# Optimization experiments

Hardware: AMD Instinct MI355X
Metric: run time of the kernel (lower is better)

## Reference

```python
import jax, jax.numpy as jnp
import numpy as np

NUM_GROUPS = 32
EPS = 1e-6


def group_norm(x, gamma, beta):
    # x: [B, C, H, W]
    b, c, h, w = x.shape
    xg = x.reshape(b, NUM_GROUPS, c // NUM_GROUPS, h, w)
    mean = xg.mean(axis=(2, 3, 4), keepdims=True)
    var = xg.var(axis=(2, 3, 4), keepdims=True)
    xn = ((xg - mean) * jax.lax.rsqrt(var + EPS)).reshape(b, c, h, w)
    return xn * gamma[None, :, None, None] + beta[None, :, None, None]


def setup_inputs() -> dict:
    key = jax.random.key(0)
    ks = jax.random.split(key, 10)
    B, C, H, W = 2, 512, 64, 64
    s = 1.0 / np.sqrt(C)
    return {
        "x": jax.random.normal(ks[0], (B, C, H, W), dtype=jnp.float32),
        "gamma": jnp.ones((C,), jnp.float32),
        "beta": jnp.zeros((C,), jnp.float32),
        "Wq": jax.random.normal(ks[1], (C, C), jnp.float32) * s,
        "bq": jnp.zeros((C,), jnp.float32),
        "Wk": jax.random.normal(ks[2], (C, C), jnp.float32) * s,
        "bk": jnp.zeros((C,), jnp.float32),
        "Wv": jax.random.normal(ks[3], (C, C), jnp.float32) * s,
        "bv": jnp.zeros((C,), jnp.float32),
        "Wo": jax.random.normal(ks[4], (C, C), jnp.float32) * s,
        "bo": jnp.zeros((C,), jnp.float32),
    }


def reference(x, gamma, beta, Wq, bq, Wk, bk, Wv, bv, Wo, bo):
    b, c, h, w = x.shape
    hn = group_norm(x, gamma, beta)               # [B,C,H,W]
    hf = hn.reshape(b, c, h * w)                  # [B,C,N]
    # 1x1 convs == channel matmuls
    q = jnp.einsum('oc,bcn->bon', Wq, hf) + bq[None, :, None]
    k = jnp.einsum('oc,bcn->bon', Wk, hf) + bk[None, :, None]
    v = jnp.einsum('oc,bcn->bon', Wv, hf) + bv[None, :, None]
    scale = float(c) ** -0.5
    scores = jnp.einsum('bci,bcj->bij', q, k) * scale   # [B,N,N]
    attn = jax.nn.softmax(scores, axis=-1)
    out = jnp.einsum('bij,bcj->bci', attn, v)            # [B,C,N]
    out = jnp.einsum('oc,bcn->bon', Wo, out) + bo[None, :, None]
    return x + out.reshape(b, c, h, w)
```

## Files before the change

### kernel.cpp

```cpp
#include <hip/hip_runtime.h>

#define BB 2
#define CC 512
#define NS 4096
#define NGROUP 32
#define TILE 128
#define RSTRIDE 132

typedef __bf16 bf16_8 __attribute__((ext_vector_type(8)));
typedef __bf16 bf16_4 __attribute__((ext_vector_type(4)));
typedef float f32_4 __attribute__((ext_vector_type(4)));

#define SMEM_BYTES 65536
#define SMEM256 131072

__device__ __forceinline__ void gld_lds16(const __bf16* g, __bf16* l) {
  __builtin_amdgcn_global_load_lds(
      (const __attribute__((address_space(1))) unsigned int*)g,
      (__attribute__((address_space(3))) unsigned int*)l, 16, 0, 0);
}

__global__ __launch_bounds__(256) void gn_stats(const float* __restrict__ x,
                                                float* __restrict__ stats) {
  const float4* p = (const float4*)(x + (size_t)blockIdx.x * 65536);
  float s = 0.f, q = 0.f;
  for (int i = threadIdx.x; i < 16384; i += 256) {
    float4 v = p[i];
    s += v.x + v.y + v.z + v.w;
    q += v.x * v.x + v.y * v.y + v.z * v.z + v.w * v.w;
  }
#pragma unroll
  for (int off = 32; off > 0; off >>= 1) {
    s += __shfl_down(s, off, 64);
    q += __shfl_down(q, off, 64);
  }
  __shared__ float ls[4], lq[4];
  int wave = threadIdx.x >> 6, lane = threadIdx.x & 63;
  if (lane == 0) { ls[wave] = s; lq[wave] = q; }
  __syncthreads();
  if (threadIdx.x == 0) {
    float S = ls[0] + ls[1] + ls[2] + ls[3];
    float Q = lq[0] + lq[1] + lq[2] + lq[3];
    float mean = S * (1.f / 65536.f);
    float var = Q * (1.f / 65536.f) - mean * mean;
    stats[blockIdx.x * 2] = mean;
    stats[blockIdx.x * 2 + 1] = rsqrtf(var + 1e-6f);
  }
}

__global__ __launch_bounds__(256) void gn_apply_t(const float* __restrict__ x,
                                                  const float* __restrict__ stats,
                                                  const float* __restrict__ gamma,
                                                  const float* __restrict__ beta,
                                                  __bf16* __restrict__ hnT) {
  __shared__ float tile[32][33];
  int b = blockIdx.z;
  int c0 = blockIdx.y * 32;
  int n0 = blockIdx.x * 32;
  int tx = threadIdx.x;
  int ty = threadIdx.y;
  const float* xb = x + (size_t)b * CC * NS;
#pragma unroll
  for (int i = 0; i < 4; i++) {
    int c = c0 + ty + i * 8;
    float mean = stats[(b * NGROUP + (c >> 4)) * 2 + 0];
    float rstd = stats[(b * NGROUP + (c >> 4)) * 2 + 1];
    float v = xb[(size_t)c * NS + n0 + tx];
    tile[ty + i * 8][tx] = (v - mean) * rstd * gamma[c] + beta[c];
  }
  __syncthreads();
  __bf16* out = hnT + (size_t)b * NS * CC;
#pragma unroll
  for (int i = 0; i < 4; i++) {
    int n = n0 + ty + i * 8;
    out[(size_t)n * CC + c0 + tx] = (__bf16)tile[tx][ty + i * 8];
  }
}

__global__ __launch_bounds__(256) void cvt_w(const float* __restrict__ w0, const float* __restrict__ w1,
                                             const float* __restrict__ w2, const float* __restrict__ w3,
                                             __bf16* __restrict__ o0, __bf16* __restrict__ o1,
                                             __bf16* __restrict__ o2, __bf16* __restrict__ o3) {
  int tsel = blockIdx.x >> 8;
  int i = (blockIdx.x & 255) * 256 + threadIdx.x;
  const float* src = tsel == 0 ? w0 : tsel == 1 ? w1 : tsel == 2 ? w2 : w3;
  __bf16* dst = tsel == 0 ? o0 : tsel == 1 ? o1 : tsel == 2 ? o2 : o3;
  float4 v = ((const float4*)src)[i];
  bf16_4 r;
  r[0] = (__bf16)v.x; r[1] = (__bf16)v.y; r[2] = (__bf16)v.z; r[3] = (__bf16)v.w;
  ((bf16_4*)dst)[i] = r;
}

__device__ __forceinline__ void gemm_core8(const __bf16* __restrict__ A, const __bf16* __restrict__ B,
                                           int K, int lda, int ldb,
                                           __bf16* lds, f32_4 (&acc)[4][2]) {
  const int t = threadIdx.x;
  const int lane = t & 63;
  const int wave = t >> 6;
  const int lrow = lane & 15, quad = lane >> 4;
  const int wrow = (wave >> 2) * 64, wcol = (wave & 3) * 32;
  const int co = (quad ^ ((lrow >> 1) & 3)) * 8;
  const int r0 = t >> 2;
  const int kp = ((t & 3) ^ ((t >> 3) & 3)) * 8;
  const __bf16* pA = A + (size_t)r0 * lda + kp;
  const __bf16* pB = B + (size_t)r0 * ldb + kp;
  {
    __bf16* lA = lds;
    __bf16* lB = lds + 8192;
    gld_lds16(pA,      &lA[t * 8]);
    gld_lds16(pA + 32, &lA[4096 + t * 8]);
    gld_lds16(pB,      &lB[t * 8]);
    gld_lds16(pB + 32, &lB[4096 + t * 8]);
  }
  int buf = 0;
  for (int k0 = 0; k0 < K; k0 += 64, buf ^= 1) {
    __syncthreads();
    if (k0 + 64 < K) {
      __bf16* lA = lds + (buf ^ 1) * 16384;
      __bf16* lB = lA + 8192;
      gld_lds16(pA + k0 + 64, &lA[t * 8]);
      gld_lds16(pA + k0 + 96, &lA[4096 + t * 8]);
      gld_lds16(pB + k0 + 64, &lB[t * 8]);
      gld_lds16(pB + k0 + 96, &lB[4096 + t * 8]);
    }
    const __bf16* bA = lds + buf * 16384;
    const __bf16* bB = bA + 8192;
#pragma unroll
    for (int ks = 0; ks < 2; ks++) {
      const __bf16* la = bA + ks * 4096;
      const __bf16* lb = bB + ks * 4096;
      bf16_8 af[4], bfr[2];
#pragma unroll
      for (int i = 0; i < 4; i++)
        af[i] = *(const bf16_8*)&la[(wrow + i * 16 + lrow) * 32 + co];
#pragma unroll
      for (int j = 0; j < 2; j++)
        bfr[j] = *(const bf16_8*)&lb[(wcol + j * 16 + lrow) * 32 + co];
#pragma unroll
      for (int i = 0; i < 4; i++)
#pragma unroll
        for (int j = 0; j < 2; j++)
          acc[i][j] = __builtin_amdgcn_mfma_f32_16x16x32_bf16(af[i], bfr[j], acc[i][j], 0, 0, 0);
    }
  }
}

__device__ __forceinline__ void stage_acc8(float* ls, const f32_4 (&acc)[4][2], int pass) {
  const int t = threadIdx.x;
  const int lane = t & 63, wave = t >> 6;
  const int lrow = lane & 15, quad = lane >> 4;
  const int wrow = (wave >> 2) * 64, wcol = (wave & 3) * 32;
  if ((wrow >> 6) == pass) {
#pragma unroll
    for (int i = 0; i < 4; i++)
#pragma unroll
      for (int r = 0; r < 4; r++)
#pragma unroll
        for (int jj = 0; jj < 2; jj++)
          ls[(i * 16 + quad * 4 + r) * RSTRIDE + wcol + jj * 16 + lrow] = acc[i][jj][r];
  }
}

__device__ __forceinline__ void drain_bf16_8(const float* ls, __bf16* gdst, int ldg) {
  const int t = threadIdx.x;
#pragma unroll
  for (int k2 = 0; k2 < 4; k2++) {
    int idx = k2 * 512 + t;
    int row = idx >> 5, col = (idx & 31) * 4;
    f32_4 v = *(const f32_4*)&ls[row * RSTRIDE + col];
    bf16_4 o;
    o[0] = (__bf16)v[0]; o[1] = (__bf16)v[1]; o[2] = (__bf16)v[2]; o[3] = (__bf16)v[3];
    *(bf16_4*)&gdst[(size_t)row * ldg + col] = o;
  }
}

__device__ __forceinline__ void gemm_core256(const __bf16* __restrict__ A,
                                             const __bf16* __restrict__ B,
                                             int K, int lda, int ldb,
                                             __bf16* lds, f32_4 (&acc)[8][4]) {
  const int t = threadIdx.x;
  const int lane = t & 63;
  const int wave = t >> 6;
  const int lrow = lane & 15, quad = lane >> 4;
  const int wm = wave >> 2, wn = wave & 3;
  const int r0 = t >> 2;
  const int kp = ((t & 3) ^ ((t >> 3) & 3)) * 8;
  const __bf16* gA0 = A + (size_t)r0 * lda + kp;
  const __bf16* gA1 = A + (size_t)(r0 + 128) * lda + kp;
  const __bf16* gB0 = B + (size_t)r0 * ldb + kp;
  const __bf16* gB1 = B + (size_t)(r0 + 128) * ldb + kp;
  const int co = (quad ^ ((lrow >> 1) & 3)) * 8;
  const int aoff = (wm * 128 + lrow) * 32 + co;
  const int boff = 16384 + (wn * 64 + lrow) * 32 + co;
  const int KT = K >> 6;

#define STG(bufv, isB, srcp, hh, ktv)                                         \
  {                                                                           \
    __bf16* d_ = lds + (bufv) * 32768 + (isB) * 16384 + (hh) * 4096 + t * 8;  \
    const __bf16* s_ = (srcp) + (ktv) * 64;                                   \
    gld_lds16(s_, d_);                                                        \
    gld_lds16(s_ + 32, d_ + 8192);                                            \
  }
#define LOAD_AF(IH)                                                           \
  _Pragma("unroll") for (int i = 0; i < 4; i++)                               \
      _Pragma("unroll") for (int ks = 0; ks < 2; ks++)                        \
          af[i][ks] = *(const bf16_8*)&bb[aoff + ((IH) * 4 + i) * 512 + ks * 8192];
#define LOAD_BV(J0)                                                           \
  _Pragma("unroll") for (int j = 0; j < 2; j++)                               \
      _Pragma("unroll") for (int ks = 0; ks < 2; ks++)                        \
          bv[(J0) + j][ks] = *(const bf16_8*)&bb[boff + ((J0) + j) * 512 + ks * 8192];
#define MFMA16(I0, J0)                                                        \
  _Pragma("unroll") for (int ks = 0; ks < 2; ks++)                            \
      _Pragma("unroll") for (int i = 0; i < 4; i++)                           \
          _Pragma("unroll") for (int j = 0; j < 2; j++)                       \
              acc[(I0) + i][(J0) + j] = __builtin_amdgcn_mfma_f32_16x16x32_bf16( \
                  af[i][ks], bv[(J0) + j][ks], acc[(I0) + i][(J0) + j], 0, 0, 0);
#define PHASE_BEGIN()                                                         \
  __builtin_amdgcn_s_barrier();                                               \
  asm volatile("s_waitcnt lgkmcnt(0)" ::: "memory");                          \
  __builtin_amdgcn_sched_barrier(0);                                          \
  __builtin_amdgcn_s_setprio(1);
#define PHASE_END()                                                           \
  __builtin_amdgcn_s_setprio(0);                                              \
  __builtin_amdgcn_s_barrier();

  STG(0, 0, gA0, 0, 0)
  STG(0, 0, gA1, 1, 0)
  STG(0, 1, gB0, 0, 0)
  STG(0, 1, gB1, 1, 0)
  STG(1, 1, gB0, 0, 1)
  STG(1, 1, gB1, 1, 1)
  asm volatile("s_waitcnt vmcnt(4)" ::: "memory");
  __builtin_amdgcn_s_barrier();

  for (int it = 0; it < (KT >> 1); ++it) {
#pragma unroll
    for (int h = 0; h < 2; ++h) {
      const int kt = 2 * it + h;
      const __bf16* bb = lds + h * 32768;
      bf16_8 af[4][2], bv[4][2];
      LOAD_AF(0)
      LOAD_BV(0)
      if (kt + 1 < KT) STG(h ^ 1, 0, gA0, 0, kt + 1)
      PHASE_BEGIN()
      MFMA16(0, 0)
      PHASE_END()
      LOAD_BV(2)
      if (kt + 1 < KT) STG(h ^ 1, 0, gA1, 1, kt + 1)
      PHASE_BEGIN()
      MFMA16(0, 2)
      PHASE_END()
      LOAD_AF(1)
      if (kt + 2 < KT) STG(h, 1, gB0, 0, kt + 2)
      PHASE_BEGIN()
      MFMA16(4, 0)
      PHASE_END()
      if (kt + 2 < KT) STG(h, 1, gB1, 1, kt + 2)
      PHASE_BEGIN()
      MFMA16(4, 2)
      __builtin_amdgcn_s_setprio(0);
      if (kt + 2 < KT) {
        asm volatile("s_waitcnt vmcnt(4)" ::: "memory");
      } else {
        asm volatile("s_waitcnt vmcnt(0)" ::: "memory");
      }
      __builtin_amdgcn_s_barrier();
    }
  }
#undef STG
#undef LOAD_AF
#undef LOAD_BV
#undef MFMA16
#undef PHASE_BEGIN
#undef PHASE_END
}

__global__ __launch_bounds__(512, 2) void e_gemm256(const __bf16* __restrict__ qT,
                                                    const __bf16* __restrict__ kT,
                                                    __bf16* __restrict__ E,
                                                    float* __restrict__ l,
                                                    float scale) {
  extern __shared__ __bf16 ldsdyn[];
  const int bid = blockIdx.x;
  const int lin = (bid & 7) * 64 + (bid >> 3);
  const int b = lin >> 8;
  const int rm = lin & 255;
  const int R = rm >> 5, s = rm & 31;
  const int mt = (R >> 2) * 8 + (s >> 2);
  const int nt = (R & 3) * 4 + (s & 3);
  const int m0 = mt * 256, n0 = nt * 256;
  const long long sBNC = (long long)NS * CC;
  const long long sBNN = (long long)NS * NS;
  const __bf16* Ap = qT + (size_t)b * sBNC + (size_t)m0 * CC;
  const __bf16* Bp = kT + (size_t)b * sBNC + (size_t)n0 * CC;

  f32_4 acc[8][4];
#pragma unroll
  for (int i = 0; i < 8; i++)
#pragma unroll
    for (int j = 0; j < 4; j++) acc[i][j] = {0.f, 0.f, 0.f, 0.f};

  gemm_core256(Ap, Bp, CC, CC, CC, ldsdyn, acc);

  const int t = threadIdx.x;
  const int lane = t & 63, wave = t >> 6;
  const int lrow = lane & 15, quad = lane >> 4;
  const int wm = wave >> 2, wn = wave & 3;
  __bf16* Ep = E + (size_t)b * sBNN;
  float* lp = l + (size_t)b * NS;
#pragma unroll
  for (int i = 0; i < 8; i++) {
#pragma unroll
    for (int r = 0; r < 4; r++) {
      int gm = m0 + wm * 128 + i * 16 + quad * 4 + r;
      float rp = 0.f;
#pragma unroll
      for (int j = 0; j < 4; j++) {
        int gn = n0 + wn * 64 + j * 16 + lrow;
        float ev = __expf(acc[i][j][r] * scale);
        rp += ev;
        Ep[(size_t)gm * NS + gn] = (__bf16)ev;
      }
      rp += __shfl_down(rp, 8, 16);
      rp += __shfl_down(rp, 4, 16);
      rp += __shfl_down(rp, 2, 16);
      rp += __shfl_down(rp, 1, 16);
      if (lrow == 0) atomicAdd(&lp[gm], rp);
    }
  }
}

__global__ __launch_bounds__(512, 2) void ao256(const __bf16* __restrict__ E,
                                                const __bf16* __restrict__ vv,
                                                __bf16* __restrict__ p0,
                                                __bf16* __restrict__ p1,
                                                __bf16* __restrict__ p2,
                                                __bf16* __restrict__ p3) {
  extern __shared__ __bf16 ldsdyn[];
  const int bid = blockIdx.x;
  const int lin = (bid & 7) * 32 + (bid >> 3);
  const int split = lin >> 6;
  const int rem = lin & 63;
  const int b = rem >> 5;
  const int mt = (rem & 31) >> 1;
  const int nt = rem & 1;
  const int m0 = mt * 256, n0 = nt * 256;
  const long long sBNN = (long long)NS * NS;
  const long long sBCN = (long long)CC * NS;
  const long long sBNC = (long long)NS * CC;
  const __bf16* Ap = E + (size_t)b * sBNN + (size_t)m0 * NS + (size_t)split * 1024;
  const __bf16* Bp = vv + (size_t)b * sBCN + (size_t)n0 * NS + (size_t)split * 1024;
  __bf16* Cp = (split == 0 ? p0 : split == 1 ? p1 : split == 2 ? p2 : p3) + (size_t)b * sBNC;

  f32_4 acc[8][4];
#pragma unroll
  for (int i = 0; i < 8; i++)
#pragma unroll
    for (int j = 0; j < 4; j++) acc[i][j] = {0.f, 0.f, 0.f, 0.f};

  gemm_core256(Ap, Bp, 1024, NS, NS, ldsdyn, acc);

  const int t = threadIdx.x;
  const int lane = t & 63, wave = t >> 6;
  const int lrow = lane & 15, quad = lane >> 4;
  const int wm = wave >> 2, wn = wave & 3;
#pragma unroll
  for (int i = 0; i < 8; i++) {
#pragma unroll
    for (int r = 0; r < 4; r++) {
      int gm = m0 + wm * 128 + i * 16 + quad * 4 + r;
#pragma unroll
      for (int j = 0; j < 4; j++) {
        int gn = n0 + wn * 64 + j * 16 + lrow;
        Cp[(size_t)gm * CC + gn] = (__bf16)acc[i][j][r];
      }
    }
  }
}

__global__ __launch_bounds__(512, 4) void qkv_gemm(const __bf16* __restrict__ hnT,
                                                   const __bf16* __restrict__ Wq,
                                                   const __bf16* __restrict__ Wk,
                                                   const __bf16* __restrict__ Wv,
                                                   const float* __restrict__ bq,
                                                   const float* __restrict__ bk,
                                                   const float* __restrict__ bv,
                                                   __bf16* __restrict__ qT,
                                                   __bf16* __restrict__ kT,
                                                   __bf16* __restrict__ vv) {
  __shared__ char smem[SMEM_BYTES];
  __bf16* lds = (__bf16*)smem;
  float* lsr = (float*)smem;
  const int b = blockIdx.z;
  const int id = blockIdx.x;
  const int sel = id >> 7;
  const int r = id & 127;
  const long long sBNC = (long long)NS * CC;
  const long long sBCN = (long long)CC * NS;

  int m0, n0, N;
  const __bf16 *Ap, *Bp;
  __bf16* Cp;
  const float* bias;
  if (sel < 2) {
    m0 = (r >> 2) * TILE;
    n0 = (r & 3) * TILE;
    Ap = hnT + (size_t)b * sBNC + (size_t)m0 * CC;
    Bp = (sel == 0 ? Wq : Wk) + (size_t)n0 * CC;
    Cp = (sel == 0 ? qT : kT) + (size_t)b * sBNC;
    bias = (sel == 0 ? bq : bk);
    N = CC;
  } else {
    m0 = (r & 3) * TILE;
    n0 = (r >> 2) * TILE;
    Ap = Wv + (size_t)m0 * CC;
    Bp = hnT + (size_t)b * sBNC + (size_t)n0 * CC;
    Cp = vv + (size_t)b * sBCN;
    bias = bv;
    N = NS;
  }

  f32_4 acc[4][2];
#pragma unroll
  for (int i = 0; i < 4; i++)
#pragma unroll
    for (int j = 0; j < 2; j++) acc[i][j] = {0.f, 0.f, 0.f, 0.f};

  gemm_core8(Ap, Bp, CC, CC, CC, lds, acc);

  const int t = threadIdx.x;
  const int lane = t & 63;
  const int lrow = lane & 15, quad = lane >> 4;
  const int wave = t >> 6;
  const int wrow = (wave >> 2) * 64, wcol = (wave & 3) * 32;
#pragma unroll
  for (int i = 0; i < 4; i++)
#pragma unroll
    for (int r2 = 0; r2 < 4; r2++) {
      float rowb = (sel == 2) ? bias[m0 + wrow + i * 16 + quad * 4 + r2] : 0.f;
#pragma unroll
      for (int j = 0; j < 2; j++) {
        float cb = (sel < 2) ? bias[n0 + wcol + j * 16 + lrow] : rowb;
        acc[i][j][r2] += cb;
      }
    }

#pragma unroll
  for (int p = 0; p < 2; p++) {
    __syncthreads();
    stage_acc8(lsr, acc, p);
    __syncthreads();
    drain_bf16_8(lsr, Cp + (size_t)(m0 + p * 64) * N + n0, N);
  }
}

__global__ __launch_bounds__(256) void reduce_ao4(const __bf16* __restrict__ p0,
                                                  const __bf16* __restrict__ p1,
                                                  const __bf16* __restrict__ p2,
                                                  const __bf16* __restrict__ p3,
                                                  const float* __restrict__ l,
                                                  __bf16* __restrict__ o) {
  int i = blockIdx.x * 256 + threadIdx.x;
  int row = i >> 6;
  float inv = 1.f / l[row];
  bf16_8 a = ((const bf16_8*)p0)[i];
  bf16_8 c = ((const bf16_8*)p1)[i];
  bf16_8 d = ((const bf16_8*)p2)[i];
  bf16_8 e = ((const bf16_8*)p3)[i];
  bf16_8 r;
#pragma unroll
  for (int k = 0; k < 8; k++)
    r[k] = (__bf16)(((float)a[k] + (float)c[k] + (float)d[k] + (float)e[k]) * inv);
  ((bf16_8*)o)[i] = r;
}

__global__ __launch_bounds__(512, 4) void wo_split(const __bf16* __restrict__ Wo,
                                                   const __bf16* __restrict__ aoT,
                                                   __bf16* __restrict__ pw0,
                                                   __bf16* __restrict__ pw1) {
  __shared__ char smem[SMEM_BYTES];
  __bf16* lds = (__bf16*)smem;
  float* lsr = (float*)smem;
  const int b = blockIdx.z & 1;
  const int split = blockIdx.z >> 1;
  const int m0 = blockIdx.y * TILE;
  const int n0 = blockIdx.x * TILE;
  const long long sBNC = (long long)NS * CC;
  const long long sBCN = (long long)CC * NS;
  const __bf16* Ap = Wo + (size_t)m0 * CC + (size_t)split * 256;
  const __bf16* Bp = aoT + (size_t)b * sBNC + (size_t)n0 * CC + (size_t)split * 256;
  __bf16* Cp = (split ? pw1 : pw0) + (size_t)b * sBCN;

  f32_4 acc[4][2];
#pragma unroll
  for (int i = 0; i < 4; i++)
#pragma unroll
    for (int j = 0; j < 2; j++) acc[i][j] = {0.f, 0.f, 0.f, 0.f};

  gemm_core8(Ap, Bp, 256, CC, CC, lds, acc);

#pragma unroll
  for (int p = 0; p < 2; p++) {
    __syncthreads();
    stage_acc8(lsr, acc, p);
    __syncthreads();
    drain_bf16_8(lsr, Cp + (size_t)(m0 + p * 64) * NS + n0, NS);
  }
}

__global__ __launch_bounds__(256) void final_out(const __bf16* __restrict__ pw0,
                                                 const __bf16* __restrict__ pw1,
                                                 const float* __restrict__ bo,
                                                 const float* __restrict__ x,
                                                 float* __restrict__ out) {
  int i = blockIdx.x * 256 + threadIdx.x;
  int o = (i >> 10) & (CC - 1);
  float bias = bo[o];
  bf16_4 a = ((const bf16_4*)pw0)[i];
  bf16_4 c = ((const bf16_4*)pw1)[i];
  float4 xr = ((const float4*)x)[i];
  float4 r;
  r.x = (float)a[0] + (float)c[0] + bias + xr.x;
  r.y = (float)a[1] + (float)c[1] + bias + xr.y;
  r.z = (float)a[2] + (float)c[2] + bias + xr.z;
  r.w = (float)a[3] + (float)c[3] + bias + xr.w;
  ((float4*)out)[i] = r;
}

extern "C" void kernel_launch(void* const* d_in, const int* in_sizes, int n_in,
                              void* d_out, int out_size, void* d_ws, size_t ws_size,
                              hipStream_t stream) {
  const float* x = (const float*)d_in[0];
  const float* gamma = (const float*)d_in[1];
  const float* beta = (const float*)d_in[2];
  const float* Wq = (const float*)d_in[3];
  const float* bq = (const float*)d_in[4];
  const float* Wk = (const float*)d_in[5];
  const float* bk = (const float*)d_in[6];
  const float* Wv = (const float*)d_in[7];
  const float* bv = (const float*)d_in[8];
  const float* Wo = (const float*)d_in[9];
  const float* bo = (const float*)d_in[10];
  float* out = (float*)d_out;

  char* ws = (char*)d_ws;
  __bf16* hnT = (__bf16*)(ws + 0);
  __bf16* qT  = (__bf16*)(ws + 8388608);
  __bf16* kT  = (__bf16*)(ws + 16777216);
  __bf16* vv  = (__bf16*)(ws + 25165824);
  __bf16* aoT = (__bf16*)(ws + 33554432);
  __bf16* Eb  = (__bf16*)(ws + 41943040);
  __bf16* pw0 = (__bf16*)(ws + 41943040);
  __bf16* pw1 = (__bf16*)(ws + 50331648);
  __bf16* Wqb = (__bf16*)(ws + 109051904);
  __bf16* Wkb = (__bf16*)(ws + 109576192);
  __bf16* Wvb = (__bf16*)(ws + 110100480);
  __bf16* Wob = (__bf16*)(ws + 110624768);
  float* stats = (float*)(ws + 111149056);
  float* lsum = (float*)(ws + 109051904);
  __bf16* p0 = hnT;
  __bf16* p1 = qT;
  __bf16* p2 = kT;
  __bf16* p3 = aoT;

  const float scale = 0.044194173824159216f;

  static int smem_attr_set = 0;
  if (!smem_attr_set) {
    hipFuncSetAttribute(reinterpret_cast<const void*>(e_gemm256),
                        hipFuncAttributeMaxDynamicSharedMemorySize, SMEM256);
    hipFuncSetAttribute(reinterpret_cast<const void*>(ao256),
                        hipFuncAttributeMaxDynamicSharedMemorySize, SMEM256);
    smem_attr_set = 1;
  }

  cvt_w<<<1024, 256, 0, stream>>>(Wq, Wk, Wv, Wo, Wqb, Wkb, Wvb, Wob);
  gn_stats<<<BB * NGROUP, 256, 0, stream>>>(x, stats);
  gn_apply_t<<<dim3(NS / 32, CC / 32, BB), dim3(32, 8), 0, stream>>>(x, stats, gamma, beta, hnT);

  qkv_gemm<<<dim3(384, 1, BB), 512, 0, stream>>>(hnT, Wqb, Wkb, Wvb, bq, bk, bv, qT, kT, vv);

  hipMemsetAsync(lsum, 0, BB * NS * sizeof(float), stream);
  e_gemm256<<<512, 512, SMEM256, stream>>>(qT, kT, Eb, lsum, scale);

  ao256<<<256, 512, SMEM256, stream>>>(Eb, vv, p0, p1, p2, p3);
  reduce_ao4<<<2048, 256, 0, stream>>>(p0, p1, p2, p3, lsum, aoT);

  wo_split<<<dim3(NS / TILE, CC / TILE, 2 * BB), 512, 0, stream>>>(Wob, aoT, pw0, pw1);
  final_out<<<4096, 256, 0, stream>>>(pw0, pw1, bo, x, out);
}
```

Measured before the change: 246.8 us.

## Use persistent two-tile E-GEMM blocks with a new K-split pipelined core

The score GEMM launches 256 blocks instead of 512. Each block computes two 256x256 output tiles that share the same Q row tile. A new GEMM core splits each 64-wide K step into two 32-wide sub-phases with double-buffered LDS and per-sub-phase barriers. This halves the block count to match the two-blocks-per-CU occupancy, so the whole grid fits in a single wave, and it spreads LDS loads across finer phases. The cost is fewer blocks, which means less latency hiding and serialised per-tile epilogues inside each block.

Result: slower. 258.4 us (+4.7%).

```diff
diff --git a/kernel.cpp b/kernel.cpp
--- a/kernel.cpp
+++ b/kernel.cpp
@@ -275,6 +275,88 @@
 #undef PHASE_END
 }
 
+__device__ __forceinline__ void gemm_core256v2(const __bf16* __restrict__ A,
+                                               const __bf16* __restrict__ B,
+                                               int K, int lda, int ldb,
+                                               __bf16* lds, f32_4 (&acc)[8][4]) {
+  const int t = threadIdx.x;
+  const int lane = t & 63;
+  const int wave = t >> 6;
+  const int lrow = lane & 15, quad = lane >> 4;
+  const int wm = wave >> 2, wn = wave & 3;
+  const int r0 = t >> 2;
+  const int kp = ((t & 3) ^ ((t >> 3) & 3)) * 8;
+  const __bf16* gA0 = A + (size_t)r0 * lda + kp;
+  const __bf16* gA1 = A + (size_t)(r0 + 128) * lda + kp;
+  const __bf16* gB0 = B + (size_t)r0 * ldb + kp;
+  const __bf16* gB1 = B + (size_t)(r0 + 128) * ldb + kp;
+  const int co = (quad ^ ((lrow >> 1) & 3)) * 8;
+  const int aoff = (wm * 128 + lrow) * 32 + co;
+  const int boff = 16384 + (wn * 64 + lrow) * 32 + co;
+  const int KT = K >> 6;
+
+#define STG4(bufv, ktv, ks)                                                    \
+  {                                                                            \
+    __bf16* dA = lds + (bufv) * 32768 + (ks) * 8192 + t * 8;                   \
+    __bf16* dB = dA + 16384;                                                   \
+    const int goff = (ktv) * 64 + (ks) * 32;                                   \
+    gld_lds16(gA0 + goff, dA);                                                 \
+    gld_lds16(gA1 + goff, dA + 4096);                                          \
+    gld_lds16(gB0 + goff, dB);                                                 \
+    gld_lds16(gB1 + goff, dB + 4096);                                          \
+  }
+#define LOAD_AF8(ks)                                                           \
+  _Pragma("unroll") for (int f = 0; f < 8; f++)                                \
+      af8[f] = *(const bf16_8*)&bb[aoff + f * 512 + (ks) * 8192];
+#define LOAD_BV4(ks)                                                           \
+  _Pragma("unroll") for (int j = 0; j < 4; j++)                                \
+      bv4[j] = *(const bf16_8*)&bb[boff + j * 512 + (ks) * 8192];
+#define MFMA32()                                                               \
+  _Pragma("unroll") for (int f = 0; f < 8; f++)                                \
+      _Pragma("unroll") for (int j = 0; j < 4; j++)                            \
+          acc[f][j] = __builtin_amdgcn_mfma_f32_16x16x32_bf16(                 \
+              af8[f], bv4[j], acc[f][j], 0, 0, 0);
+#define PHASE2(h, kt, ks)                                                      \
+  {                                                                            \
+    const __bf16* bb = lds + (h) * 32768;                                      \
+    bf16_8 af8[8], bv4[4];                                                     \
+    LOAD_AF8(ks)                                                               \
+    LOAD_BV4(ks)                                                               \
+    if ((kt) + 1 < KT) STG4((h) ^ 1, (kt) + 1, ks)                             \
+    asm volatile("s_waitcnt lgkmcnt(8)" ::: "memory");                         \
+    __builtin_amdgcn_s_barrier();                                              \
+    asm volatile("s_waitcnt lgkmcnt(0)" ::: "memory");                         \
+    __builtin_amdgcn_sched_barrier(0);                                         \
+    __builtin_amdgcn_s_setprio(1);                                             \
+    MFMA32()                                                                   \
+    __builtin_amdgcn_s_setprio(0);                                             \
+    if ((kt) + 1 < KT) {                                                       \
+      asm volatile("s_waitcnt vmcnt(4)" ::: "memory");                         \
+    } else if ((ks) == 0) {                                                    \
+      asm volatile("s_waitcnt vmcnt(0)" ::: "memory");                         \
+    }                                                                          \
+    __builtin_amdgcn_s_barrier();                                              \
+  }
+
+  STG4(0, 0, 0)
+  STG4(0, 0, 1)
+  asm volatile("s_waitcnt vmcnt(4)" ::: "memory");
+  __builtin_amdgcn_s_barrier();
+
+  for (int it = 0; it < (KT >> 1); ++it) {
+    const int kt0 = 2 * it;
+    PHASE2(0, kt0, 0)
+    PHASE2(0, kt0, 1)
+    PHASE2(1, kt0 + 1, 0)
+    PHASE2(1, kt0 + 1, 1)
+  }
+#undef STG4
+#undef LOAD_AF8
+#undef LOAD_BV4
+#undef MFMA32
+#undef PHASE2
+}
+
 __global__ __launch_bounds__(512, 2) void e_gemm256(const __bf16* __restrict__ qT,
                                                     const __bf16* __restrict__ kT,
                                                     __bf16* __restrict__ E,
@@ -282,50 +364,55 @@
                                                     float scale) {
   extern __shared__ __bf16 ldsdyn[];
   const int bid = blockIdx.x;
-  const int lin = (bid & 7) * 64 + (bid >> 3);
-  const int b = lin >> 8;
-  const int rm = lin & 255;
-  const int R = rm >> 5, s = rm & 31;
-  const int mt = (R >> 2) * 8 + (s >> 2);
-  const int nt = (R & 3) * 4 + (s & 3);
-  const int m0 = mt * 256, n0 = nt * 256;
+  const int lin = (bid & 7) * 32 + (bid >> 3);
+  const int b = lin >> 7;
+  const int rm = lin & 127;
+  const int mt = rm >> 3;
+  const int np = rm & 7;
+  const int m0 = mt * 256;
   const long long sBNC = (long long)NS * CC;
   const long long sBNN = (long long)NS * NS;
   const __bf16* Ap = qT + (size_t)b * sBNC + (size_t)m0 * CC;
-  const __bf16* Bp = kT + (size_t)b * sBNC + (size_t)n0 * CC;
-
-  f32_4 acc[8][4];
-#pragma unroll
-  for (int i = 0; i < 8; i++)
-#pragma unroll
-    for (int j = 0; j < 4; j++) acc[i][j] = {0.f, 0.f, 0.f, 0.f};
-
-  gemm_core256(Ap, Bp, CC, CC, CC, ldsdyn, acc);
+  __bf16* Ep = E + (size_t)b * sBNN;
+  float* lp = l + (size_t)b * NS;
 
   const int t = threadIdx.x;
   const int lane = t & 63, wave = t >> 6;
   const int lrow = lane & 15, quad = lane >> 4;
   const int wm = wave >> 2, wn = wave & 3;
-  __bf16* Ep = E + (size_t)b * sBNN;
-  float* lp = l + (size_t)b * NS;
-#pragma unroll
-  for (int i = 0; i < 8; i++) {
-#pragma unroll
-    for (int r = 0; r < 4; r++) {
-      int gm = m0 + wm * 128 + i * 16 + quad * 4 + r;
-      float rp = 0.f;
-#pragma unroll
-      for (int j = 0; j < 4; j++) {
-        int gn = n0 + wn * 64 + j * 16 + lrow;
-        float ev = __expf(acc[i][j][r] * scale);
-        rp += ev;
-        Ep[(size_t)gm * NS + gn] = (__bf16)ev;
+
+#pragma unroll
+  for (int half = 0; half < 2; ++half) {
+    const int n0 = (np + half * 8) * 256;
+    const __bf16* Bp = kT + (size_t)b * sBNC + (size_t)n0 * CC;
+
+    f32_4 acc[8][4];
+#pragma unroll
+    for (int i = 0; i < 8; i++)
+#pragma unroll
+      for (int j = 0; j < 4; j++) acc[i][j] = {0.f, 0.f, 0.f, 0.f};
+
+    gemm_core256v2(Ap, Bp, CC, CC, CC, ldsdyn, acc);
+
+#pragma unroll
+    for (int i = 0; i < 8; i++) {
+#pragma unroll
+      for (int r = 0; r < 4; r++) {
+        int gm = m0 + wm * 128 + i * 16 + quad * 4 + r;
+        float rp = 0.f;
+#pragma unroll
+        for (int j = 0; j < 4; j++) {
+          int gn = n0 + wn * 64 + j * 16 + lrow;
+          float ev = __expf(acc[i][j][r] * scale);
+          rp += ev;
+          Ep[(size_t)gm * NS + gn] = (__bf16)ev;
+        }
+        rp += __shfl_down(rp, 8, 16);
+        rp += __shfl_down(rp, 4, 16);
+        rp += __shfl_down(rp, 2, 16);
+        rp += __shfl_down(rp, 1, 16);
+        if (lrow == 0) atomicAdd(&lp[gm], rp);
       }
-      rp += __shfl_down(rp, 8, 16);
-      rp += __shfl_down(rp, 4, 16);
-      rp += __shfl_down(rp, 2, 16);
-      rp += __shfl_down(rp, 1, 16);
-      if (lrow == 0) atomicAdd(&lp[gm], rp);
     }
   }
 }
@@ -581,7 +668,7 @@
   qkv_gemm<<<dim3(384, 1, BB), 512, 0, stream>>>(hnT, Wqb, Wkb, Wvb, bq, bk, bv, qT, kT, vv);
 
   hipMemsetAsync(lsum, 0, BB * NS * sizeof(float), stream);
-  e_gemm256<<<512, 512, SMEM256, stream>>>(qT, kT, Eb, lsum, scale);
+  e_gemm256<<<256, 512, SMEM256, stream>>>(qT, kT, Eb, lsum, scale);
 
   ao256<<<256, 512, SMEM256, stream>>>(Eb, vv, p0, p1, p2, p3);
   reduce_ao4<<<2048, 256, 0, stream>>>(p0, p1, p2, p3, lsum, aoT);
```

## Replace 256x256 score GEMM with 256x128 tiles and triple-buffered LDS pipeline

Applied to the files above, without the earlier changes.

The exp(QK^T) score kernel moves from 256x256 output tiles with a 128KB LDS footprint to 256x128 tiles. A new GEMM core triple-buffers 32-wide K slices in 72KB of LDS, and launch bounds rise to 4 blocks per CU with twice as many blocks. The aim is higher occupancy and better latency hiding for a K=512 GEMM that is dominated by its epilogue. The cost is lower per-block reuse of the K operand, more redundant loads of Q, and tighter register budgets.

Measured after the change: 260.1 us. +5.4%, slower.

```diff
diff --git a/kernel.cpp b/kernel.cpp
--- a/kernel.cpp
+++ b/kernel.cpp
@@ -13,6 +13,7 @@
 
 #define SMEM_BYTES 65536
 #define SMEM256 131072
+#define SMEM_E 73728
 
 __device__ __forceinline__ void gld_lds16(const __bf16* g, __bf16* l) {
   __builtin_amdgcn_global_load_lds(
@@ -275,44 +276,111 @@
 #undef PHASE_END
 }
 
-__global__ __launch_bounds__(512, 2) void e_gemm256(const __bf16* __restrict__ qT,
-                                                    const __bf16* __restrict__ kT,
-                                                    __bf16* __restrict__ E,
-                                                    float* __restrict__ l,
-                                                    float scale) {
+__device__ __forceinline__ void gemm_coreE(const __bf16* __restrict__ A,
+                                           const __bf16* __restrict__ B,
+                                           int K, int lda, int ldb,
+                                           __bf16* lds, f32_4 (&acc)[4][4]) {
+  const int t = threadIdx.x;
+  const int lane = t & 63;
+  const int wave = t >> 6;
+  const int lrow = lane & 15, quad = lane >> 4;
+  const int wm = wave >> 1, wn = wave & 1;
+  const int r0 = t >> 2;
+  const int kp = ((t & 3) ^ ((t >> 3) & 3)) * 8;
+  const __bf16* gA0 = A + (size_t)r0 * lda + kp;
+  const __bf16* gA1 = A + (size_t)(r0 + 128) * lda + kp;
+  const __bf16* gB0 = B + (size_t)r0 * ldb + kp;
+  const int co = (quad ^ ((lrow >> 1) & 3)) * 8;
+  const int aoff = (wm * 64 + lrow) * 32 + co;
+  const int boff = 8192 + (wn * 64 + lrow) * 32 + co;
+  const int KT = K >> 5;
+
+  __bf16* cb  = lds;
+  __bf16* nb1 = lds + 12288;
+  __bf16* nb2 = lds + 24576;
+
+  {
+    __bf16* d = cb + t * 8;
+    gld_lds16(gA0, d);
+    gld_lds16(gA1, d + 4096);
+    gld_lds16(gB0, d + 8192);
+    d = nb1 + t * 8;
+    gld_lds16(gA0 + 32, d);
+    gld_lds16(gA1 + 32, d + 4096);
+    gld_lds16(gB0 + 32, d + 8192);
+  }
+  asm volatile("s_waitcnt vmcnt(3)" ::: "memory");
+  __builtin_amdgcn_s_barrier();
+
+  for (int kt = 0; kt < KT; ++kt) {
+    bf16_8 af[4], bv[4];
+#pragma unroll
+    for (int i = 0; i < 4; i++) af[i] = *(const bf16_8*)&cb[aoff + i * 512];
+#pragma unroll
+    for (int j = 0; j < 4; j++) bv[j] = *(const bf16_8*)&cb[boff + j * 512];
+    if (kt + 2 < KT) {
+      const int go = (kt + 2) * 32;
+      __bf16* d = nb2 + t * 8;
+      gld_lds16(gA0 + go, d);
+      gld_lds16(gA1 + go, d + 4096);
+      gld_lds16(gB0 + go, d + 8192);
+      asm volatile("s_waitcnt vmcnt(3)" ::: "memory");
+    } else {
+      asm volatile("s_waitcnt vmcnt(0)" ::: "memory");
+    }
+    __builtin_amdgcn_s_barrier();
+    asm volatile("s_waitcnt lgkmcnt(0)" ::: "memory");
+    __builtin_amdgcn_sched_barrier(0);
+    __builtin_amdgcn_s_setprio(1);
+#pragma unroll
+    for (int i = 0; i < 4; i++)
+#pragma unroll
+      for (int j = 0; j < 4; j++)
+        acc[i][j] = __builtin_amdgcn_mfma_f32_16x16x32_bf16(af[i], bv[j], acc[i][j], 0, 0, 0);
+    __builtin_amdgcn_s_setprio(0);
+    __builtin_amdgcn_s_barrier();
+    __bf16* tmp = cb; cb = nb1; nb1 = nb2; nb2 = tmp;
+  }
+}
+
+__global__ __launch_bounds__(512, 4) void e_gemmE(const __bf16* __restrict__ qT,
+                                                  const __bf16* __restrict__ kT,
+                                                  __bf16* __restrict__ E,
+                                                  float* __restrict__ l,
+                                                  float scale) {
   extern __shared__ __bf16 ldsdyn[];
   const int bid = blockIdx.x;
-  const int lin = (bid & 7) * 64 + (bid >> 3);
-  const int b = lin >> 8;
-  const int rm = lin & 255;
-  const int R = rm >> 5, s = rm & 31;
-  const int mt = (R >> 2) * 8 + (s >> 2);
-  const int nt = (R & 3) * 4 + (s & 3);
-  const int m0 = mt * 256, n0 = nt * 256;
+  const int lin = (bid & 7) * 128 + (bid >> 3);
+  const int b = lin >> 9;
+  const int rm = lin & 511;
+  const int g = rm >> 6, s = rm & 63;
+  const int mt = (g & 1) * 8 + (s >> 3);
+  const int nt = (g >> 1) * 8 + (s & 7);
+  const int m0 = mt * 256, n0 = nt * 128;
   const long long sBNC = (long long)NS * CC;
   const long long sBNN = (long long)NS * NS;
   const __bf16* Ap = qT + (size_t)b * sBNC + (size_t)m0 * CC;
   const __bf16* Bp = kT + (size_t)b * sBNC + (size_t)n0 * CC;
 
-  f32_4 acc[8][4];
-#pragma unroll
-  for (int i = 0; i < 8; i++)
+  f32_4 acc[4][4];
+#pragma unroll
+  for (int i = 0; i < 4; i++)
 #pragma unroll
     for (int j = 0; j < 4; j++) acc[i][j] = {0.f, 0.f, 0.f, 0.f};
 
-  gemm_core256(Ap, Bp, CC, CC, CC, ldsdyn, acc);
+  gemm_coreE(Ap, Bp, CC, CC, CC, ldsdyn, acc);
 
   const int t = threadIdx.x;
   const int lane = t & 63, wave = t >> 6;
   const int lrow = lane & 15, quad = lane >> 4;
-  const int wm = wave >> 2, wn = wave & 3;
+  const int wm = wave >> 1, wn = wave & 1;
   __bf16* Ep = E + (size_t)b * sBNN;
   float* lp = l + (size_t)b * NS;
 #pragma unroll
-  for (int i = 0; i < 8; i++) {
+  for (int i = 0; i < 4; i++) {
 #pragma unroll
     for (int r = 0; r < 4; r++) {
-      int gm = m0 + wm * 128 + i * 16 + quad * 4 + r;
+      int gm = m0 + wm * 64 + i * 16 + quad * 4 + r;
       float rp = 0.f;
 #pragma unroll
       for (int j = 0; j < 4; j++) {
@@ -567,8 +635,8 @@
 
   static int smem_attr_set = 0;
   if (!smem_attr_set) {
-    hipFuncSetAttribute(reinterpret_cast<const void*>(e_gemm256),
-                        hipFuncAttributeMaxDynamicSharedMemorySize, SMEM256);
+    hipFuncSetAttribute(reinterpret_cast<const void*>(e_gemmE),
+                        hipFuncAttributeMaxDynamicSharedMemorySize, SMEM_E);
     hipFuncSetAttribute(reinterpret_cast<const void*>(ao256),
                         hipFuncAttributeMaxDynamicSharedMemorySize, SMEM256);
     smem_attr_set = 1;
@@ -581,7 +649,7 @@
   qkv_gemm<<<dim3(384, 1, BB), 512, 0, stream>>>(hnT, Wqb, Wkb, Wvb, bq, bk, bv, qT, kT, vv);
 
   hipMemsetAsync(lsum, 0, BB * NS * sizeof(float), stream);
-  e_gemm256<<<512, 512, SMEM256, stream>>>(qT, kT, Eb, lsum, scale);
+  e_gemmE<<<1024, 512, SMEM_E, stream>>>(qT, kT, Eb, lsum, scale);
 
   ao256<<<256, 512, SMEM256, stream>>>(Eb, vv, p0, p1, p2, p3);
   reduce_ao4<<<2048, 256, 0, stream>>>(p0, p1, p2, p3, lsum, aoT);
```

## Use simpler double-buffered GEMM core for scores and drop split-K in Wo projection

Applied to the files above, without the earlier changes.

Adds a new GEMM mainloop, gemm_coreF, for the QK^T score kernel. It double-buffers 64-wide K tiles loaded straight into LDS with a swizzled layout and uses one barrier per iteration, replacing the earlier phase-scheduled core. Separately, the output projection now runs the full K=512 in one kernel instead of two split-K halves. This removes the second partial buffer and its extra read in final_out, at the cost of half as many blocks in that GEMM.

Result: no change. 242.4 us (-1.8%).

```diff
diff --git a/kernel.cpp b/kernel.cpp
--- a/kernel.cpp
+++ b/kernel.cpp
@@ -275,6 +275,71 @@
 #undef PHASE_END
 }
 
+__device__ __forceinline__ void gemm_coreF(const __bf16* __restrict__ A,
+                                           const __bf16* __restrict__ B,
+                                           int K, int lda, int ldb,
+                                           __bf16* lds, f32_4 (&acc)[8][4]) {
+  const int t = threadIdx.x;
+  const int lane = t & 63;
+  const int wave = t >> 6;
+  const int lrow = lane & 15, quad = lane >> 4;
+  const int wm = wave >> 2, wn = wave & 3;
+  const int r0 = t >> 2;
+  const int kp = ((t & 3) ^ ((t >> 3) & 3)) * 8;
+  const __bf16* gA0 = A + (size_t)r0 * lda + kp;
+  const __bf16* gA1 = A + (size_t)(r0 + 128) * lda + kp;
+  const __bf16* gB0 = B + (size_t)r0 * ldb + kp;
+  const __bf16* gB1 = B + (size_t)(r0 + 128) * ldb + kp;
+  const int co = (quad ^ ((lrow >> 1) & 3)) * 8;
+  const int aoff = (wm * 128 + lrow) * 32 + co;
+  const int boff = 16384 + (wn * 64 + lrow) * 32 + co;
+  const int KT = K >> 6;
+
+  {
+    __bf16* d = lds + t * 8;
+    gld_lds16(gA0,      d);
+    gld_lds16(gA1,      d + 4096);
+    gld_lds16(gA0 + 32, d + 8192);
+    gld_lds16(gA1 + 32, d + 12288);
+    gld_lds16(gB0,      d + 16384);
+    gld_lds16(gB1,      d + 20480);
+    gld_lds16(gB0 + 32, d + 24576);
+    gld_lds16(gB1 + 32, d + 28672);
+  }
+  int buf = 0;
+  for (int kt = 0; kt < KT; ++kt, buf ^= 1) {
+    __syncthreads();
+    if (kt + 1 < KT) {
+      __bf16* d = lds + (buf ^ 1) * 32768 + t * 8;
+      const int go = (kt + 1) * 64;
+      gld_lds16(gA0 + go,      d);
+      gld_lds16(gA1 + go,      d + 4096);
+      gld_lds16(gA0 + go + 32, d + 8192);
+      gld_lds16(gA1 + go + 32, d + 12288);
+      gld_lds16(gB0 + go,      d + 16384);
+      gld_lds16(gB1 + go,      d + 20480);
+      gld_lds16(gB0 + go + 32, d + 24576);
+      gld_lds16(gB1 + go + 32, d + 28672);
+    }
+    const __bf16* bb = lds + buf * 32768;
+#pragma unroll
+    for (int ks = 0; ks < 2; ks++) {
+      bf16_8 af[8], bv[4];
+#pragma unroll
+      for (int f = 0; f < 8; f++)
+        af[f] = *(const bf16_8*)&bb[aoff + f * 512 + ks * 8192];
+#pragma unroll
+      for (int j = 0; j < 4; j++)
+        bv[j] = *(const bf16_8*)&bb[boff + j * 512 + ks * 8192];
+#pragma unroll
+      for (int f = 0; f < 8; f++)
+#pragma unroll
+        for (int j = 0; j < 4; j++)
+          acc[f][j] = __builtin_amdgcn_mfma_f32_16x16x32_bf16(af[f], bv[j], acc[f][j], 0, 0, 0);
+    }
+  }
+}
+
 __global__ __launch_bounds__(512, 2) void e_gemm256(const __bf16* __restrict__ qT,
                                                     const __bf16* __restrict__ kT,
                                                     __bf16* __restrict__ E,
@@ -300,7 +365,7 @@
 #pragma unroll
     for (int j = 0; j < 4; j++) acc[i][j] = {0.f, 0.f, 0.f, 0.f};
 
-  gemm_core256(Ap, Bp, CC, CC, CC, ldsdyn, acc);
+  gemm_coreF(Ap, Bp, CC, CC, CC, ldsdyn, acc);
 
   const int t = threadIdx.x;
   const int lane = t & 63, wave = t >> 6;
@@ -474,22 +539,20 @@
   ((bf16_8*)o)[i] = r;
 }
 
-__global__ __launch_bounds__(512, 4) void wo_split(const __bf16* __restrict__ Wo,
-                                                   const __bf16* __restrict__ aoT,
-                                                   __bf16* __restrict__ pw0,
-                                                   __bf16* __restrict__ pw1) {
+__global__ __launch_bounds__(512, 4) void wo_full(const __bf16* __restrict__ Wo,
+                                                  const __bf16* __restrict__ aoT,
+                                                  __bf16* __restrict__ pw0) {
   __shared__ char smem[SMEM_BYTES];
   __bf16* lds = (__bf16*)smem;
   float* lsr = (float*)smem;
-  const int b = blockIdx.z & 1;
-  const int split = blockIdx.z >> 1;
+  const int b = blockIdx.z;
   const int m0 = blockIdx.y * TILE;
   const int n0 = blockIdx.x * TILE;
   const long long sBNC = (long long)NS * CC;
   const long long sBCN = (long long)CC * NS;
-  const __bf16* Ap = Wo + (size_t)m0 * CC + (size_t)split * 256;
-  const __bf16* Bp = aoT + (size_t)b * sBNC + (size_t)n0 * CC + (size_t)split * 256;
-  __bf16* Cp = (split ? pw1 : pw0) + (size_t)b * sBCN;
+  const __bf16* Ap = Wo + (size_t)m0 * CC;
+  const __bf16* Bp = aoT + (size_t)b * sBNC + (size_t)n0 * CC;
+  __bf16* Cp = pw0 + (size_t)b * sBCN;
 
   f32_4 acc[4][2];
 #pragma unroll
@@ -497,7 +560,7 @@
 #pragma unroll
     for (int j = 0; j < 2; j++) acc[i][j] = {0.f, 0.f, 0.f, 0.f};
 
-  gemm_core8(Ap, Bp, 256, CC, CC, lds, acc);
+  gemm_core8(Ap, Bp, CC, CC, CC, lds, acc);
 
 #pragma unroll
   for (int p = 0; p < 2; p++) {
@@ -509,7 +572,6 @@
 }
 
 __global__ __launch_bounds__(256) void final_out(const __bf16* __restrict__ pw0,
-                                                 const __bf16* __restrict__ pw1,
                                                  const float* __restrict__ bo,
                                                  const float* __restrict__ x,
                                                  float* __restrict__ out) {
@@ -517,13 +579,12 @@
   int o = (i >> 10) & (CC - 1);
   float bias = bo[o];
   bf16_4 a = ((const bf16_4*)pw0)[i];
-  bf16_4 c = ((const bf16_4*)pw1)[i];
   float4 xr = ((const float4*)x)[i];
   float4 r;
-  r.x = (float)a[0] + (float)c[0] + bias + xr.x;
-  r.y = (float)a[1] + (float)c[1] + bias + xr.y;
-  r.z = (float)a[2] + (float)c[2] + bias + xr.z;
-  r.w = (float)a[3] + (float)c[3] + bias + xr.w;
+  r.x = (float)a[0] + bias + xr.x;
+  r.y = (float)a[1] + bias + xr.y;
+  r.z = (float)a[2] + bias + xr.z;
+  r.w = (float)a[3] + bias + xr.w;
   ((float4*)out)[i] = r;
 }
 
@@ -551,7 +612,6 @@
   __bf16* aoT = (__bf16*)(ws + 33554432);
   __bf16* Eb  = (__bf16*)(ws + 41943040);
   __bf16* pw0 = (__bf16*)(ws + 41943040);
-  __bf16* pw1 = (__bf16*)(ws + 50331648);
   __bf16* Wqb = (__bf16*)(ws + 109051904);
   __bf16* Wkb = (__bf16*)(ws + 109576192);
   __bf16* Wvb = (__bf16*)(ws + 110100480);
@@ -586,6 +646,6 @@
   ao256<<<256, 512, SMEM256, stream>>>(Eb, vv, p0, p1, p2, p3);
   reduce_ao4<<<2048, 256, 0, stream>>>(p0, p1, p2, p3, lsum, aoT);
 
-  wo_split<<<dim3(NS / TILE, CC / TILE, 2 * BB), 512, 0, stream>>>(Wob, aoT, pw0, pw1);
-  final_out<<<4096, 256, 0, stream>>>(pw0, pw1, bo, x, out);
-}
+  wo_full<<<dim3(NS / TILE, CC / TILE, BB), 512, 0, stream>>>(Wob, aoT, pw0);
+  final_out<<<4096, 256, 0, stream>>>(pw0, bo, x, out);
+}
```
